# Optimization experiments

Measured on AMD Instinct MI355X. Metric: run time of the kernel, lower is better.

Reference implementation:

```python
import jax, jax.numpy as jnp
import numpy as np

NUM_BLOCKS = 256
BLOCK_SIZE = 256
BATCH = 16
MAX_BLOCKS = 8            # max_context_len = MAX_BLOCKS * BLOCK_SIZE = 2048
NUM_HEADS = 32
NUM_KV_HEADS = 8
HEAD_DIM = 128
SCALE = 1.0 / np.sqrt(HEAD_DIM).astype(np.float32)


def setup_inputs() -> dict:
    key = jax.random.key(0)
    ks = jax.random.split(key, 5)
    q = jax.random.normal(ks[0], (BATCH, NUM_HEADS, HEAD_DIM), dtype=jnp.float32)
    k = jax.random.normal(ks[1], (BATCH, NUM_KV_HEADS, HEAD_DIM), dtype=jnp.float32)
    v = jax.random.normal(ks[2], (BATCH, NUM_KV_HEADS, HEAD_DIM), dtype=jnp.float32)
    k_cache = jax.random.normal(ks[3], (NUM_BLOCKS, BLOCK_SIZE, NUM_KV_HEADS, HEAD_DIM), dtype=jnp.float32)
    v_cache = jax.random.normal(ks[4], (NUM_BLOCKS, BLOCK_SIZE, NUM_KV_HEADS, HEAD_DIM), dtype=jnp.float32)
    rng = np.random.default_rng(0)
    # distinct blocks per sequence (16*8 = 128 <= 256 available blocks)
    block_tables = rng.permutation(NUM_BLOCKS)[: BATCH * MAX_BLOCKS].reshape(BATCH, MAX_BLOCKS).astype(np.int32)
    context_lens = rng.integers(1, MAX_BLOCKS * BLOCK_SIZE + 1, size=(BATCH,)).astype(np.int32)
    pos = context_lens - 1  # slot of the token being written this decode step
    slot_mapping = (block_tables[np.arange(BATCH), pos // BLOCK_SIZE] * BLOCK_SIZE + pos % BLOCK_SIZE).astype(np.int32)
    return {
        "q": q, "k": k, "v": v,
        "k_cache": k_cache, "v_cache": v_cache,
        "block_tables": jnp.asarray(block_tables),
        "context_lens": jnp.asarray(context_lens),
        "slot_mapping": jnp.asarray(slot_mapping),
    }


def _store_kv(key_t, value_t, kc_flat, vc_flat, slot_mapping):
    # scatter new K/V tokens to cache slots; slot < 0 means skip
    valid = slot_mapping >= 0
    safe = jnp.where(valid, slot_mapping, 0)
    kc_flat = kc_flat.at[safe].set(jnp.where(valid[:, None, None], key_t, kc_flat[safe]))
    vc_flat = vc_flat.at[safe].set(jnp.where(valid[:, None, None], value_t, vc_flat[safe]))
    return kc_flat, vc_flat


def reference(q, k, v, k_cache, v_cache, block_tables, context_lens, slot_mapping):
    # 1) store current-step K/V to paged cache (flattened view)
    kc_flat = k_cache.reshape(-1, NUM_KV_HEADS, HEAD_DIM)
    vc_flat = v_cache.reshape(-1, NUM_KV_HEADS, HEAD_DIM)
    kc_flat, vc_flat = _store_kv(k, v, kc_flat, vc_flat, slot_mapping)
    kc = kc_flat.reshape(NUM_BLOCKS, BLOCK_SIZE, NUM_KV_HEADS, HEAD_DIM)
    vc = vc_flat.reshape(NUM_BLOCKS, BLOCK_SIZE, NUM_KV_HEADS, HEAD_DIM)

    # 2) gather K/V blocks per sequence -> [B, L, KV, D], L = MAX_BLOCKS*BLOCK_SIZE
    safe_bt = jnp.clip(block_tables, 0, NUM_BLOCKS - 1)
    L = MAX_BLOCKS * BLOCK_SIZE
    k_g = kc[safe_bt.reshape(-1)].reshape(BATCH, L, NUM_KV_HEADS, HEAD_DIM)
    v_g = vc[safe_bt.reshape(-1)].reshape(BATCH, L, NUM_KV_HEADS, HEAD_DIM)
    kv_mask = jnp.arange(L)[None, :] < context_lens[:, None]  # [B, L]

    # 3) grouped-query attention, one query token per sequence
    G = NUM_HEADS // NUM_KV_HEADS
    q_g = q.reshape(BATCH, NUM_KV_HEADS, G, HEAD_DIM)
    scores = jnp.einsum('bkgd,blkd->bkgl', q_g, k_g) * SCALE  # [B, KV, G, L]
    scores = jnp.where(kv_mask[:, None, None, :], scores, -1e9)
    w = jax.nn.softmax(scores, axis=-1)
    out = jnp.einsum('bkgl,blkd->bkgd', w, v_g)
    return out.reshape(BATCH, NUM_HEADS, HEAD_DIM)
```

## Files before the change

kernel.cpp:

```cpp
#include <hip/hip_runtime.h>

#define BATCH 16
#define NUM_HEADS 32
#define NUM_KV 8
#define GQ 4
#define HD 128
#define PAGE 256
#define MAXB 8
#define NS 8
#define TPS 256
#define QSCALE 0.08838834764831845f

#define WS_STRIDE 520

template <int CTRL>
__device__ __forceinline__ float dpp_add(float x) {
  int xi = __builtin_bit_cast(int, x);
  int yi = __builtin_amdgcn_update_dpp(0, xi, CTRL, 0xF, 0xF, true);
  return x + __builtin_bit_cast(float, yi);
}
__device__ __forceinline__ float red16(float x) {
  x = dpp_add<0xB1>(x);
  x = dpp_add<0x4E>(x);
  x = dpp_add<0x141>(x);
  x = dpp_add<0x140>(x);
  return x;
}

__global__ __launch_bounds__(256) void pa_partial(
    const float* __restrict__ q,
    const float* __restrict__ knew,
    const float* __restrict__ vnew,
    const float* __restrict__ kc,
    const float* __restrict__ vc,
    const int* __restrict__ block_tables,
    const int* __restrict__ context_lens,
    float* __restrict__ ws)
{
  int blk = blockIdx.x;
  int t = blk >> 8;
  int r = blk & 255;
  int b = (t << 2) | (r & 3);
  int kvh = (r >> 2) & 7;
  int split = ((r >> 5) + (t << 1)) & 7;

  int ctx = context_lens[b];
  int start = split * TPS;
  if (start >= ctx) return;
  int n = min(TPS, ctx - start);
  int page = block_tables[b * MAXB + split];
  int pbase = page * PAGE;

  int tid = threadIdx.x;
  int w = tid >> 6;
  int lane = tid & 63;
  int grp = lane >> 4;
  int j = lane & 15;
  int tb = w * 4 + grp;

  __shared__ float s_l[4][GQ];
  __shared__ float s_acc[4][GQ][HD];

  float qr[GQ][8];
  #pragma unroll
  for (int g = 0; g < GQ; ++g) {
    const float* qp = q + ((size_t)(b * NUM_HEADS + kvh * GQ + g)) * HD;
    float4 a = *(const float4*)(qp + j * 4);
    float4 c = *(const float4*)(qp + 64 + j * 4);
    qr[g][0]=a.x*QSCALE; qr[g][1]=a.y*QSCALE; qr[g][2]=a.z*QSCALE; qr[g][3]=a.w*QSCALE;
    qr[g][4]=c.x*QSCALE; qr[g][5]=c.y*QSCALE; qr[g][6]=c.z*QSCALE; qr[g][7]=c.w*QSCALE;
  }

  const float* knew_row = knew + (size_t)(b * NUM_KV + kvh) * HD + j * 4;
  const float* vnew_row = vnew + (size_t)(b * NUM_KV + kvh) * HD + j * 4;
  size_t base_off = ((size_t)pbase * NUM_KV + kvh) * HD + j * 4;
  const float* kbase = kc + base_off;
  const float* vbase = vc + base_off;
  int newpos = ctx - 1 - start;
  bool hasnew = (newpos >= 0) && (newpos < n);

  int iters = (n + 15) >> 4;

  float l[GQ] = {0.f, 0.f, 0.f, 0.f};
  float acc[GQ][8];
  #pragma unroll
  for (int g = 0; g < GQ; ++g)
    #pragma unroll
    for (int e = 0; e < 8; ++e) acc[g][e] = 0.f;

  #pragma unroll 2
  for (int i = 0; i < iters; ++i) {
    int tl = tb + i * 16;
    int tlc = (tl < n) ? tl : 0;
    size_t off = (size_t)tlc * (NUM_KV * HD);
    float4 k0 = *(const float4*)(kbase + off);
    float4 k1 = *(const float4*)(kbase + off + 64);
    float4 v0 = *(const float4*)(vbase + off);
    float4 v1 = *(const float4*)(vbase + off + 64);
    float kk[8] = {k0.x,k0.y,k0.z,k0.w,k1.x,k1.y,k1.z,k1.w};
    float vv[8] = {v0.x,v0.y,v0.z,v0.w,v1.x,v1.y,v1.z,v1.w};
    float s0 = 0.f, s1 = 0.f, s2 = 0.f, s3 = 0.f;
    #pragma unroll
    for (int e = 0; e < 8; ++e) {
      s0 += qr[0][e] * kk[e];
      s1 += qr[1][e] * kk[e];
      s2 += qr[2][e] * kk[e];
      s3 += qr[3][e] * kk[e];
    }
    s0 = red16(s0);
    s1 = red16(s1);
    s2 = red16(s2);
    s3 = red16(s3);
    if (tl < n) {
      float p0 = __expf(fminf(s0, 60.f));
      float p1 = __expf(fminf(s1, 60.f));
      float p2 = __expf(fminf(s2, 60.f));
      float p3 = __expf(fminf(s3, 60.f));
      l[0] += p0; l[1] += p1; l[2] += p2; l[3] += p3;
      #pragma unroll
      for (int e = 0; e < 8; ++e) {
        acc[0][e] += p0 * vv[e];
        acc[1][e] += p1 * vv[e];
        acc[2][e] += p2 * vv[e];
        acc[3][e] += p3 * vv[e];
      }
    }
  }

  if (hasnew && tid < 16) {
    size_t off = (size_t)newpos * (NUM_KV * HD);
    float4 k0 = *(const float4*)(kbase + off);
    float4 k1 = *(const float4*)(kbase + off + 64);
    float4 v0 = *(const float4*)(vbase + off);
    float4 v1 = *(const float4*)(vbase + off + 64);
    float ks[8] = {k0.x,k0.y,k0.z,k0.w,k1.x,k1.y,k1.z,k1.w};
    float vs[8] = {v0.x,v0.y,v0.z,v0.w,v1.x,v1.y,v1.z,v1.w};
    float4 nk0 = *(const float4*)(knew_row);
    float4 nk1 = *(const float4*)(knew_row + 64);
    float4 nv0 = *(const float4*)(vnew_row);
    float4 nv1 = *(const float4*)(vnew_row + 64);
    float kn[8] = {nk0.x,nk0.y,nk0.z,nk0.w,nk1.x,nk1.y,nk1.z,nk1.w};
    float vn[8] = {nv0.x,nv0.y,nv0.z,nv0.w,nv1.x,nv1.y,nv1.z,nv1.w};
    #pragma unroll
    for (int g = 0; g < GQ; ++g) {
      float ss = 0.f, sn = 0.f;
      #pragma unroll
      for (int e = 0; e < 8; ++e) {
        ss += qr[g][e] * ks[e];
        sn += qr[g][e] * kn[e];
      }
      ss = red16(ss);
      sn = red16(sn);
      float ps = __expf(fminf(ss, 60.f));
      float pn = __expf(fminf(sn, 60.f));
      l[g] += pn - ps;
      #pragma unroll
      for (int e = 0; e < 8; ++e) acc[g][e] += pn * vn[e] - ps * vs[e];
    }
  }

  #pragma unroll
  for (int g = 0; g < GQ; ++g) {
    #pragma unroll
    for (int e = 0; e < 8; ++e) {
      acc[g][e] += __shfl_xor(acc[g][e], 16);
      acc[g][e] += __shfl_xor(acc[g][e], 32);
    }
    l[g] += __shfl_xor(l[g], 16);
    l[g] += __shfl_xor(l[g], 32);
  }
  if (lane < 16) {
    #pragma unroll
    for (int g = 0; g < GQ; ++g) {
      #pragma unroll
      for (int e = 0; e < 4; ++e) s_acc[w][g][j * 4 + e] = acc[g][e];
      #pragma unroll
      for (int e = 4; e < 8; ++e) s_acc[w][g][64 + j * 4 + e - 4] = acc[g][e];
    }
  }
  if (lane == 0) {
    #pragma unroll
    for (int g = 0; g < GQ; ++g) s_l[w][g] = l[g];
  }
  __syncthreads();

  float* outp = ws + (size_t)(((b * NUM_KV) + kvh) * NS + split) * WS_STRIDE;
  #pragma unroll
  for (int idx = tid; idx < GQ * HD; idx += 256) {
    int g = idx >> 7;
    int d = idx & 127;
    float A = s_acc[0][g][d] + s_acc[1][g][d] + s_acc[2][g][d] + s_acc[3][g][d];
    outp[8 + idx] = A;
    if (d == 0) {
      outp[g] = s_l[0][g] + s_l[1][g] + s_l[2][g] + s_l[3][g];
    }
  }
}

__global__ __launch_bounds__(128) void pa_reduce(
    const float* __restrict__ ws,
    const int* __restrict__ context_lens,
    float* __restrict__ out)
{
  int blk = blockIdx.x;
  int g  = blk & 3;
  int kv = (blk >> 2) & 7;
  int b  = blk >> 5;
  int d  = threadIdx.x;
  int ctx = context_lens[b];
  int ns = (ctx + TPS - 1) / TPS;
  const float* base = ws + (size_t)((b * NUM_KV + kv) * NS) * WS_STRIDE;

  float Lsum = 0.f, A = 0.f;
  for (int s = 0; s < ns; ++s) {
    Lsum += base[s * WS_STRIDE + g];
    A    += base[s * WS_STRIDE + 8 + g * HD + d];
  }
  out[((size_t)(b * NUM_HEADS) + kv * GQ + g) * HD + d] = A / Lsum;
}

extern "C" void kernel_launch(void* const* d_in, const int* in_sizes, int n_in,
                              void* d_out, int out_size, void* d_ws, size_t ws_size,
                              hipStream_t stream) {
  const float* q  = (const float*)d_in[0];
  const float* k  = (const float*)d_in[1];
  const float* v  = (const float*)d_in[2];
  const float* kc = (const float*)d_in[3];
  const float* vc = (const float*)d_in[4];
  const int* block_tables = (const int*)d_in[5];
  const int* context_lens = (const int*)d_in[6];

  float* ws = (float*)d_ws;
  float* out = (float*)d_out;

  pa_partial<<<BATCH * NUM_KV * NS, 256, 0, stream>>>(
      q, k, v, kc, vc, block_tables, context_lens, ws);
  pa_reduce<<<BATCH * NUM_KV * GQ, 128, 0, stream>>>(ws, context_lens, out);
}
```

Baseline: 34.12 us.

## Load-balance split-K pieces across sequences by total context length

```diff
diff --git a/kernel.cpp b/kernel.cpp
--- a/kernel.cpp
+++ b/kernel.cpp
@@ -7,9 +7,9 @@
 #define HD 128
 #define PAGE 256
 #define MAXB 8
-#define NS 8
-#define TPS 256
+#define SLOTS 8
 #define QSCALE 0.08838834764831845f
+#define ROWSZ (NUM_KV * HD)
 
 #define WS_STRIDE 520
 
@@ -25,6 +25,18 @@
   x = dpp_add<0x141>(x);
   x = dpp_add<0x140>(x);
   return x;
+}
+
+__device__ __forceinline__ int piece_P(const int* __restrict__ context_lens,
+                                       int cx[BATCH]) {
+  int total = 0;
+  #pragma unroll
+  for (int bb = 0; bb < BATCH; ++bb) { cx[bb] = context_lens[bb]; total += cx[bb]; }
+  return (total + 63) >> 6;
+}
+__device__ __forceinline__ int piece_nb(int ctx, int P) {
+  int nb = (ctx + (P >> 1)) / P;
+  return nb < 1 ? 1 : (nb > SLOTS ? SLOTS : nb);
 }
 
 __global__ __launch_bounds__(256) void pa_partial(
@@ -37,19 +49,26 @@
     const int* __restrict__ context_lens,
     float* __restrict__ ws)
 {
+  int cx[BATCH];
+  int P = piece_P(context_lens, cx);
+
   int blk = blockIdx.x;
-  int t = blk >> 8;
-  int r = blk & 255;
-  int b = (t << 2) | (r & 3);
-  int kvh = (r >> 2) & 7;
-  int split = ((r >> 5) + (t << 1)) & 7;
-
-  int ctx = context_lens[b];
-  int start = split * TPS;
+  int b = -1, local = 0, acc_ = 0;
+  #pragma unroll
+  for (int bb = 0; bb < BATCH; ++bb) {
+    int np = piece_nb(cx[bb], P) * NUM_KV;
+    if (b < 0 && blk < acc_ + np) { b = bb; local = blk - acc_; }
+    acc_ += np;
+  }
+  if (b < 0) return;
+  int ctx = cx[b];
+  int nb = piece_nb(ctx, P);
+  int sz = (ctx + nb - 1) / nb;
+  int kvh = local & 7;
+  int piece = local >> 3;
+  int start = piece * sz;
   if (start >= ctx) return;
-  int n = min(TPS, ctx - start);
-  int page = block_tables[b * MAXB + split];
-  int pbase = page * PAGE;
+  int n = min(sz, ctx - start);
 
   int tid = threadIdx.x;
   int w = tid >> 6;
@@ -58,8 +77,10 @@
   int j = lane & 15;
   int tb = w * 4 + grp;
 
+  __shared__ int s_pg[MAXB];
   __shared__ float s_l[4][GQ];
   __shared__ float s_acc[4][GQ][HD];
+  if (tid < MAXB) s_pg[tid] = block_tables[b * MAXB + tid];
 
   float qr[GQ][8];
   #pragma unroll
@@ -70,14 +91,15 @@
     qr[g][0]=a.x*QSCALE; qr[g][1]=a.y*QSCALE; qr[g][2]=a.z*QSCALE; qr[g][3]=a.w*QSCALE;
     qr[g][4]=c.x*QSCALE; qr[g][5]=c.y*QSCALE; qr[g][6]=c.z*QSCALE; qr[g][7]=c.w*QSCALE;
   }
+  __syncthreads();
 
   const float* knew_row = knew + (size_t)(b * NUM_KV + kvh) * HD + j * 4;
   const float* vnew_row = vnew + (size_t)(b * NUM_KV + kvh) * HD + j * 4;
-  size_t base_off = ((size_t)pbase * NUM_KV + kvh) * HD + j * 4;
-  const float* kbase = kc + base_off;
-  const float* vbase = vc + base_off;
-  int newpos = ctx - 1 - start;
-  bool hasnew = (newpos >= 0) && (newpos < n);
+  size_t lane_off = (size_t)kvh * HD + j * 4;
+  const float* kbase = kc + lane_off;
+  const float* vbase = vc + lane_off;
+  int newloc = ctx - 1 - start;
+  bool hasnew = (newloc >= 0) && (newloc < n);
 
   int iters = (n + 15) >> 4;
 
@@ -92,7 +114,9 @@
   for (int i = 0; i < iters; ++i) {
     int tl = tb + i * 16;
     int tlc = (tl < n) ? tl : 0;
-    size_t off = (size_t)tlc * (NUM_KV * HD);
+    int tok = start + tlc;
+    int row = s_pg[tok >> 8] * PAGE + (tok & (PAGE - 1));
+    size_t off = (size_t)row * ROWSZ;
     float4 k0 = *(const float4*)(kbase + off);
     float4 k1 = *(const float4*)(kbase + off + 64);
     float4 v0 = *(const float4*)(vbase + off);
@@ -128,7 +152,9 @@
   }
 
   if (hasnew && tid < 16) {
-    size_t off = (size_t)newpos * (NUM_KV * HD);
+    int tokn = ctx - 1;
+    int rown = s_pg[tokn >> 8] * PAGE + (tokn & (PAGE - 1));
+    size_t off = (size_t)rown * ROWSZ;
     float4 k0 = *(const float4*)(kbase + off);
     float4 k1 = *(const float4*)(kbase + off + 64);
     float4 v0 = *(const float4*)(vbase + off);
@@ -184,7 +210,7 @@
   }
   __syncthreads();
 
-  float* outp = ws + (size_t)(((b * NUM_KV) + kvh) * NS + split) * WS_STRIDE;
+  float* outp = ws + (size_t)(((b * NUM_KV) + kvh) * SLOTS + piece) * WS_STRIDE;
   #pragma unroll
   for (int idx = tid; idx < GQ * HD; idx += 256) {
     int g = idx >> 7;
@@ -202,17 +228,19 @@
     const int* __restrict__ context_lens,
     float* __restrict__ out)
 {
+  int cx[BATCH];
+  int P = piece_P(context_lens, cx);
+
   int blk = blockIdx.x;
   int g  = blk & 3;
   int kv = (blk >> 2) & 7;
   int b  = blk >> 5;
   int d  = threadIdx.x;
-  int ctx = context_lens[b];
-  int ns = (ctx + TPS - 1) / TPS;
-  const float* base = ws + (size_t)((b * NUM_KV + kv) * NS) * WS_STRIDE;
+  int nb = piece_nb(cx[b], P);
+  const float* base = ws + (size_t)((b * NUM_KV + kv) * SLOTS) * WS_STRIDE;
 
   float Lsum = 0.f, A = 0.f;
-  for (int s = 0; s < ns; ++s) {
+  for (int s = 0; s < nb; ++s) {
     Lsum += base[s * WS_STRIDE + g];
     A    += base[s * WS_STRIDE + 8 + g * HD + d];
   }
@@ -233,7 +261,7 @@
   float* ws = (float*)d_ws;
   float* out = (float*)d_out;
 
-  pa_partial<<<BATCH * NUM_KV * NS, 256, 0, stream>>>(
+  pa_partial<<<1024, 256, 0, stream>>>(
       q, k, v, kc, vc, block_tables, context_lens, ws);
   pa_reduce<<<BATCH * NUM_KV * GQ, 128, 0, stream>>>(ws, context_lens, out);
 }
```

Measured after the change: 40.50 us. 18.7% more time.
